# Optimization experiments

Measured on AMD Instinct MI355X. Metric: run time of the kernel, lower is better.

Reference implementation:

```python
import jax, jax.numpy as jnp
import numpy as np

CODEBOOK_SIZE = 65536
HIDDEN = 768
B, L = 2, 2048
COMMITMENT_COST = 0.25


def setup_inputs() -> dict:
    key = jax.random.key(0)
    k1, k2 = jax.random.split(key)
    embeddings = jax.random.normal(k1, (B, L, HIDDEN), dtype=jnp.float32)
    # torch init: uniform(-1/K, 1/K)
    bound = 1.0 / CODEBOOK_SIZE
    codebook = jax.random.uniform(k2, (CODEBOOK_SIZE, HIDDEN), dtype=jnp.float32,
                                  minval=-bound, maxval=bound)
    return {"embeddings": embeddings, "codebook": codebook}


def reference(embeddings, codebook):
    Bv, Lv, D = embeddings.shape
    z = embeddings.reshape(-1, D)  # (N, D)
    # pairwise squared distances: z^2 + e^2 - 2 z e^T  -> (N, K)
    z_sq = jnp.sum(z * z, axis=-1, keepdims=True)          # (N, 1)
    e_sq = jnp.sum(codebook * codebook, axis=-1)[None, :]  # (1, K)
    distances = z_sq + e_sq - 2.0 * (z @ codebook.T)       # (N, K)
    codes = jnp.argmin(distances, axis=-1)                 # (N,)
    quantized = codebook[codes]                            # (N, D) gather
    # VQ loss: codebook loss + commitment loss (stop-grads as in torch .detach())
    codebook_loss = jnp.mean((quantized - jax.lax.stop_gradient(z)) ** 2)
    commitment_loss = jnp.mean((z - jax.lax.stop_gradient(quantized)) ** 2)
    vq_loss = codebook_loss + COMMITMENT_COST * commitment_loss
    # straight-through estimator
    quantized_ste = z + jax.lax.stop_gradient(quantized - z)
    return (codes.reshape(Bv, Lv),
            quantized_ste.reshape(Bv, Lv, D),
            vq_loss)
```

## Files before the change

### kernel.cpp

```cpp
#include <hip/hip_runtime.h>
#include <cfloat>
#include <cstdint>

#define NROWS  4096
#define DIM    768
#define KCODES 65536

#define TM 128
#define TC 128
#define BK 64
#define SA 40
#define CAP 2048
#define DELTA 3.0e-4f

#define WS_ZSQ    0
#define WS_RUNMIN 16384
#define WS_CNT    32768
#define WS_CODESI 49152
#define WS_LOSS   65536
#define WS_LIST   131072
#define WS_AH     (WS_LIST + (size_t)NROWS*CAP*4)
#define WS_BH     (WS_AH + (size_t)NROWS*DIM*2)
#define WS_NEED   (WS_BH + (size_t)KCODES*DIM*2)

typedef _Float16 half_t;
typedef _Float16 half4 __attribute__((ext_vector_type(4)));
typedef _Float16 half8 __attribute__((ext_vector_type(8)));
typedef float    f32x4 __attribute__((ext_vector_type(4)));
typedef unsigned int uint;
typedef __attribute__((address_space(3))) half_t lds_half_t;

__device__ __forceinline__ void gld16(half_t* lds, const half_t* g) {
  __builtin_amdgcn_global_load_lds(
      (const __attribute__((address_space(1))) unsigned int*)g,
      (__attribute__((address_space(3))) unsigned int*)lds, 16, 0, 0);
}

__global__ void k_convA(const float* __restrict__ z, half_t* __restrict__ h,
                        float* __restrict__ zsq, unsigned int* __restrict__ runmin,
                        int* __restrict__ cnt, double* __restrict__ loss) {
  const int wave = threadIdx.x >> 6, lane = threadIdx.x & 63;
  const int row = blockIdx.x * 4 + wave;
  const float4* zr = (const float4*)(z + (size_t)row * DIM);
  half_t* hr = h + (size_t)row * DIM;
  float s = 0.f;
  #pragma unroll
  for (int p = 0; p < 3; ++p) {
    float4 v = zr[lane + p * 64];
    s = fmaf(v.x, v.x, s); s = fmaf(v.y, v.y, s);
    s = fmaf(v.z, v.z, s); s = fmaf(v.w, v.w, s);
    half4 hv = { (half_t)v.x, (half_t)v.y, (half_t)v.z, (half_t)v.w };
    *(half4*)(hr + (lane + p * 64) * 4) = hv;
  }
  #pragma unroll
  for (int off = 32; off; off >>= 1) s += __shfl_xor(s, off, 64);
  if (lane == 0) zsq[row] = s;
  const int gid = blockIdx.x * 256 + threadIdx.x;
  if (gid < NROWS) { runmin[gid] = 0x7f7fffffu; cnt[gid] = 0; }
  if (gid == 0) *loss = 0.0;
}

__global__ void k_convB(const float* __restrict__ src, half_t* __restrict__ h, int n8) {
  const int i = blockIdx.x * 256 + threadIdx.x;
  if (i >= n8) return;
  float4 v0 = ((const float4*)src)[2 * i];
  float4 v1 = ((const float4*)src)[2 * i + 1];
  float a[8] = {v0.x, v0.y, v0.z, v0.w, v1.x, v1.y, v1.z, v1.w};
  half8 hi;
  #pragma unroll
  for (int j = 0; j < 8; ++j) hi[j] = (half_t)(a[j] * 4096.f);
  ((half8*)h)[i] = hi;
}


#define GATE4 asm volatile("s_waitcnt vmcnt(4)" ::: "memory")
#define GATE0 asm volatile("s_waitcnt vmcnt(0)" ::: "memory")
#define GATEN
#define NOSTAGE

#define DSR(dst, base, imm) \
  asm volatile("ds_read_b128 %0, %1 offset:%2" : "=v"(dst) : "v"(base), "n"(imm))

#define MFMA2(AI, Ax0, Ax1, Bx0, Bx1) \
  acc[AI] = __builtin_amdgcn_mfma_f32_16x16x32_f16(Ax0, Bx0, acc[AI], 0, 0, 0); \
  acc[AI] = __builtin_amdgcn_mfma_f32_16x16x32_f16(Ax1, Bx1, acc[AI], 0, 0, 0)

#define STAGE_A(BUF, H, KD) { \
  gld16(stA + (BUF)*16384 + ((H)*128 +  0)*64, gAbase + (size_t)(((H)*64 +   0)*DIM) + (KD)); \
  gld16(stA + (BUF)*16384 + ((H)*128 + 64)*64, gAbase + (size_t)(((H)*64 + 128)*DIM) + (KD)); }

#define STAGE_B(BUF, G, KD) { \
  gld16(stB + (BUF)*16384 + ((G)*128 +  0)*64, gBbase + (size_t)(((G)*32 +   0)*DIM) + (KD)); \
  gld16(stB + (BUF)*16384 + ((G)*128 + 64)*64, gBbase + (size_t)(((G)*32 + 128)*DIM) + (KD)); }

#define PHASE_BODY(BUF, H, G, STAGE, GATE) { \
  half8 a00, a10, a20, a30, a01, a11, a21, a31, b00, b10, b01, b11; \
  DSR(a00, rA##BUF##0, (H)*16384 + 0); \
  DSR(a10, rA##BUF##0, (H)*16384 + 2048); \
  DSR(a20, rA##BUF##0, (H)*16384 + 4096); \
  DSR(a30, rA##BUF##0, (H)*16384 + 6144); \
  DSR(a01, rA##BUF##1, (H)*16384 + 0); \
  DSR(a11, rA##BUF##1, (H)*16384 + 2048); \
  DSR(a21, rA##BUF##1, (H)*16384 + 4096); \
  DSR(a31, rA##BUF##1, (H)*16384 + 6144); \
  DSR(b00, rB##BUF##0, (G)*16384 + 0); \
  DSR(b10, rB##BUF##0, (G)*16384 + 2048); \
  DSR(b01, rB##BUF##1, (G)*16384 + 0); \
  DSR(b11, rB##BUF##1, (G)*16384 + 2048); \
  STAGE; \
  __builtin_amdgcn_s_barrier(); \
  asm volatile("s_waitcnt lgkmcnt(0)" ::: "memory"); \
  __builtin_amdgcn_sched_barrier(0); \
  __builtin_amdgcn_s_setprio(1); \
  MFMA2(((H)*4+0)*4 + (G)*2 + 0, a00, a01, b00, b01); \
  MFMA2(((H)*4+0)*4 + (G)*2 + 1, a00, a01, b10, b11); \
  MFMA2(((H)*4+1)*4 + (G)*2 + 0, a10, a11, b00, b01); \
  MFMA2(((H)*4+1)*4 + (G)*2 + 1, a10, a11, b10, b11); \
  MFMA2(((H)*4+2)*4 + (G)*2 + 0, a20, a21, b00, b01); \
  MFMA2(((H)*4+2)*4 + (G)*2 + 1, a20, a21, b10, b11); \
  MFMA2(((H)*4+3)*4 + (G)*2 + 0, a30, a31, b00, b01); \
  MFMA2(((H)*4+3)*4 + (G)*2 + 1, a30, a31, b10, b11); \
  __builtin_amdgcn_s_setprio(0); \
  GATE; \
  __builtin_amdgcn_s_barrier(); }

__global__ __launch_bounds__(512, 2) void k1_s1(
    const half_t* __restrict__ Ahg, const half_t* __restrict__ Bhg,
    const float* __restrict__ zsq, unsigned int* __restrict__ runmin,
    int* __restrict__ cnt, int* __restrict__ list) {
  __shared__ __align__(16) half_t sA[2][256 * 64];
  __shared__ __align__(16) half_t sB[2][256 * 64];
  __shared__ float lzs[256];
  __shared__ float redD[256][4];
  __shared__ float lbound[256];

  const int tid = threadIdx.x;
  const int row0  = blockIdx.x * 256;
  const int code0 = blockIdx.y * 256;
  const int wave = tid >> 6, lane = tid & 63;
  const int wm = wave >> 2, wn = wave & 3;
  const int q = lane >> 4, l16 = lane & 15;
  const int sr = lane >> 3, ss = lane & 7;
  const int gsw8 = (ss ^ sr) * 8;
  const int s0 = wave * 8 + sr;

  if (tid < 256) lzs[tid] = zsq[row0 + tid];

  const uint ldsA = (uint)(size_t)(lds_half_t*)&sA[0][0];
  const uint ldsB = (uint)(size_t)(lds_half_t*)&sB[0][0];
  const int xr = l16 & 7;
  const uint rA00 = ldsA + (uint)((wm * 64 + l16) * 128 + ((q ^ xr) * 16));
  const uint rA01 = ldsA + (uint)((wm * 64 + l16) * 128 + (((4 + q) ^ xr) * 16));
  const uint rA10 = rA00 + 32768u;
  const uint rA11 = rA01 + 32768u;
  const uint rB00 = ldsB + (uint)((wn * 32 + l16) * 128 + ((q ^ xr) * 16));
  const uint rB01 = ldsB + (uint)((wn * 32 + l16) * 128 + (((4 + q) ^ xr) * 16));
  const uint rB10 = rB00 + 32768u;
  const uint rB11 = rB01 + 32768u;

  half_t* stA = &sA[0][0] + s0 * 64 + ss * 8;
  half_t* stB = &sB[0][0] + s0 * 64 + ss * 8;
  const half_t* gAbase = Ahg + (size_t)(row0 + s0) * DIM + gsw8;
  const half_t* gBbase = Bhg + (size_t)(code0 + (s0 >> 5) * 64 + (s0 & 31)) * DIM + gsw8;

  f32x4 acc[32];
  #pragma unroll
  for (int i = 0; i < 32; ++i) acc[i] = (f32x4){0.f, 0.f, 0.f, 0.f};

  STAGE_A(0, 0, 0);  STAGE_B(0, 1, 0);  STAGE_A(0, 1, 0);  STAGE_B(0, 0, 0);
  STAGE_A(1, 0, 64); STAGE_B(1, 1, 64);
  GATE4;
  asm volatile("s_waitcnt lgkmcnt(0)" ::: "memory");
  __builtin_amdgcn_s_barrier();

  for (int t = 0; t < 5; ++t) {
    const int kdB  = t * 128 + 64;
    const int kdN0 = t * 128 + 128;
    const int kdN1 = t * 128 + 192;
    PHASE_BODY(0, 0, 0, STAGE_A(1, 1, kdB),  GATEN);
    PHASE_BODY(0, 0, 1, STAGE_B(1, 0, kdB),  GATEN);
    PHASE_BODY(0, 1, 1, STAGE_A(0, 0, kdN0), GATEN);
    PHASE_BODY(0, 1, 0, STAGE_B(0, 1, kdN0), GATE4);
    PHASE_BODY(1, 0, 0, STAGE_A(0, 1, kdN0), GATEN);
    PHASE_BODY(1, 0, 1, STAGE_B(0, 0, kdN0), GATEN);
    PHASE_BODY(1, 1, 1, STAGE_A(1, 0, kdN1), GATEN);
    PHASE_BODY(1, 1, 0, STAGE_B(1, 1, kdN1), GATE4);
  }
  {
    PHASE_BODY(0, 0, 0, STAGE_A(1, 1, 704), GATEN);
    PHASE_BODY(0, 0, 1, STAGE_B(1, 0, 704), GATEN);
    PHASE_BODY(0, 1, 1, NOSTAGE, GATEN);
    PHASE_BODY(0, 1, 0, NOSTAGE, GATE0);
    PHASE_BODY(1, 0, 0, NOSTAGE, GATEN);
    PHASE_BODY(1, 0, 1, NOSTAGE, GATEN);
    PHASE_BODY(1, 1, 1, NOSTAGE, GATEN);
    PHASE_BODY(1, 1, 0, NOSTAGE, GATEN);
  }

  const float c2 = -4.8828125e-4f;
  #pragma unroll
  for (int tm = 0; tm < 8; ++tm)
    #pragma unroll
    for (int reg = 0; reg < 4; ++reg) {
      const float zs = lzs[wm * 128 + tm * 16 + q * 4 + reg];
      #pragma unroll
      for (int tn = 0; tn < 4; ++tn)
        acc[tm * 4 + tn][reg] = fmaf(c2, acc[tm * 4 + tn][reg], zs);
    }

  #pragma unroll
  for (int tm = 0; tm < 8; ++tm)
    #pragma unroll
    for (int reg = 0; reg < 4; ++reg) {
      float m = acc[tm * 4 + 0][reg];
      #pragma unroll
      for (int tn = 1; tn < 4; ++tn) m = fminf(m, acc[tm * 4 + tn][reg]);
      #pragma unroll
      for (int off = 8; off; off >>= 1) m = fminf(m, __shfl_xor(m, off, 64));
      if (l16 == 0) redD[wm * 128 + tm * 16 + q * 4 + reg][wn] = m;
    }
  __syncthreads();
  if (tid < 256) {
    const float lm = fminf(fminf(redD[tid][0], redD[tid][1]),
                           fminf(redD[tid][2], redD[tid][3]));
    const unsigned rg = runmin[row0 + tid];
    atomicMin(&runmin[row0 + tid], __float_as_uint(lm));
    lbound[tid] = fminf(lm, __uint_as_float(rg)) + DELTA;
  }
  __syncthreads();

  #pragma unroll
  for (int tm = 0; tm < 8; ++tm)
    #pragma unroll
    for (int reg = 0; reg < 4; ++reg) {
      const int row_b = wm * 128 + tm * 16 + q * 4 + reg;
      const float b = lbound[row_b];
      #pragma unroll
      for (int tn = 0; tn < 4; ++tn) {
        const float d = acc[tm * 4 + tn][reg];
        if (d <= b) {
          const int grow = row0 + row_b;
          const int pos = atomicAdd(&cnt[grow], 1);
          if (pos < CAP) list[(size_t)grow * CAP + pos] = code0 + wn * 64 + tn * 16 + l16;
        }
      }
    }
}

__global__ void k_refine(const float* __restrict__ z, const float* __restrict__ cb,
                         const float* __restrict__ zsq, const int* __restrict__ cnt,
                         const int* __restrict__ list, float* __restrict__ out_codes,
                         float* __restrict__ outq, double* __restrict__ loss) {
  const int r = blockIdx.x;
  const int tid = threadIdx.x, wave = tid >> 6, lane = tid & 63;
  __shared__ unsigned long long wbest[4];
  __shared__ double wsum[4];
  __shared__ int sidx;
  __shared__ __align__(16) float zsh[DIM];

  if (tid < DIM / 4) ((float4*)zsh)[tid] = ((const float4*)(z + (size_t)r * DIM))[tid];
  __syncthreads();

  int n = cnt[r]; if (n > CAP) n = CAP;
  const bool empty = (n == 0); if (empty) n = 1;
  const double zsd = (double)zsq[r];
  unsigned long long best = ~0ull;
  for (int ci = wave; ci < n; ci += 4) {
    const int idx = empty ? 0 : list[(size_t)r * CAP + ci];
    const float4* cr = (const float4*)(cb + (size_t)idx * DIM);
    double s = 0.0;
    #pragma unroll
    for (int p = 0; p < 3; ++p) {
      const float4 cv = cr[lane + p * 64];
      const float4 zv = ((const float4*)zsh)[lane + p * 64];
      s += (double)zv.x * cv.x + (double)zv.y * cv.y +
           (double)zv.z * cv.z + (double)zv.w * cv.w;
    }
    #pragma unroll
    for (int off = 32; off; off >>= 1) s += __shfl_xor(s, off, 64);
    const float d = (float)(zsd - 2.0 * s);
    const unsigned long long key =
        ((unsigned long long)__float_as_uint(d) << 32) | (unsigned)idx;
    if (key < best) best = key;
  }
  if (lane == 0) wbest[wave] = best;
  __syncthreads();
  if (tid == 0) {
    unsigned long long b = wbest[0];
    #pragma unroll
    for (int w = 1; w < 4; ++w) if (wbest[w] < b) b = wbest[w];
    const int idx = (int)(unsigned)(b & 0xffffffffull);
    sidx = idx;
    out_codes[r] = (float)idx;
  }
  __syncthreads();

  const int c = sidx;
  double ls = 0.0;
  #pragma unroll
  for (int j = 0; j < 3; ++j) {
    const int e = tid + j * 256;
    const float qx = cb[(size_t)c * DIM + e];
    const float zx = zsh[e];
    const float dd = qx - zx;
    outq[(size_t)r * DIM + e] = zx + dd;
    ls += (double)dd * (double)dd;
  }
  #pragma unroll
  for (int off = 32; off; off >>= 1) ls += __shfl_xor(ls, off, 64);
  if (lane == 0) wsum[wave] = ls;
  __syncthreads();
  if (tid == 0) atomicAdd(loss, wsum[0] + wsum[1] + wsum[2] + wsum[3]);
}

__global__ void k4_final(const double* __restrict__ loss, float* __restrict__ out) {
  float m = (float)(*loss / ((double)NROWS * (double)DIM));
  out[0] = m + 0.25f * m;
}

__global__ void k0_zsq(const float* __restrict__ z, float* __restrict__ zsq,
                       unsigned long long* __restrict__ keys, double* __restrict__ loss) {
  const int wave = threadIdx.x >> 6, lane = threadIdx.x & 63;
  const int row = blockIdx.x * 4 + wave;
  const float* zr = z + (size_t)row * DIM;
  float s = 0.f;
  #pragma unroll
  for (int i = 0; i < DIM / 64; ++i) { float v = zr[lane + i * 64]; s = fmaf(v, v, s); }
  #pragma unroll
  for (int off = 32; off; off >>= 1) s += __shfl_xor(s, off, 64);
  if (lane == 0) zsq[row] = s;
  const int gid = blockIdx.x * 256 + threadIdx.x;
  if (gid < NROWS) keys[gid] = ~0ull;
  if (gid == 0) *loss = 0.0;
}

__global__ __launch_bounds__(256, 2) void k1_mfma(
    const float* __restrict__ z, const float* __restrict__ cb,
    const float* __restrict__ zsq, unsigned long long* __restrict__ keys) {
  __shared__ half_t Ah[TM * SA], Al[TM * SA], Bh[TC * SA], Bl[TC * SA];
  __shared__ float lzs[TM];
  __shared__ float redD[TM][2];
  __shared__ int   redI[TM][2];

  const int tid  = threadIdx.x;
  const int row0  = blockIdx.x * TM;
  const int code0 = blockIdx.y * TC;
  const int wave = tid >> 6, lane = tid & 63;
  const int wm = wave & 1, wn = wave >> 1;
  const int q = lane >> 4, l16 = lane & 15;

  if (tid < TM) lzs[tid] = zsq[row0 + tid];

  const int srow = tid >> 2;
  const int sko  = (tid & 3) * 8;

  f32x4 acc0[16], acc1[16];
  #pragma unroll
  for (int i = 0; i < 16; ++i) {
    acc0[i] = (f32x4){0.f, 0.f, 0.f, 0.f};
    acc1[i] = (f32x4){0.f, 0.f, 0.f, 0.f};
  }

  const float* zp = z  + (size_t)row0  * DIM;
  const float* bp = cb + (size_t)code0 * DIM;

  for (int kd = 0; kd < DIM; kd += 32) {
    __syncthreads();
    #pragma unroll
    for (int s = 0; s < 2; ++s) {
      const int r = srow + s * 64;
      const float* srca = zp + (size_t)r * DIM + kd + sko;
      float4 v0 = *(const float4*)srca;
      float4 v1 = *(const float4*)(srca + 4);
      float a[8] = {v0.x, v0.y, v0.z, v0.w, v1.x, v1.y, v1.z, v1.w};
      half8 hi, lo;
      #pragma unroll
      for (int j = 0; j < 8; ++j) {
        half_t h = (half_t)a[j];
        hi[j] = h;
        lo[j] = (half_t)((a[j] - (float)h) * 4096.f);
      }
      *(half8*)&Ah[r * SA + sko] = hi;
      *(half8*)&Al[r * SA + sko] = lo;
      const float* srcb = bp + (size_t)r * DIM + kd + sko;
      v0 = *(const float4*)srcb; v1 = *(const float4*)(srcb + 4);
      float b[8] = {v0.x, v0.y, v0.z, v0.w, v1.x, v1.y, v1.z, v1.w};
      #pragma unroll
      for (int j = 0; j < 8; ++j) {
        float bs = b[j] * 4096.f;
        half_t h = (half_t)bs;
        hi[j] = h;
        lo[j] = (half_t)((bs - (float)h) * 4096.f);
      }
      *(half8*)&Bh[r * SA + sko] = hi;
      *(half8*)&Bl[r * SA + sko] = lo;
    }
    __syncthreads();

    half8 fa_h[4], fa_l[4], fb_h[4], fb_l[4];
    #pragma unroll
    for (int t = 0; t < 4; ++t) {
      const int ar = (wm * 64 + t * 16 + l16) * SA + q * 8;
      fa_h[t] = *(const half8*)&Ah[ar];
      fa_l[t] = *(const half8*)&Al[ar];
      const int br = (wn * 64 + t * 16 + l16) * SA + q * 8;
      fb_h[t] = *(const half8*)&Bh[br];
      fb_l[t] = *(const half8*)&Bl[br];
    }
    #pragma unroll
    for (int tm = 0; tm < 4; ++tm)
      #pragma unroll
      for (int tn = 0; tn < 4; ++tn) {
        const int i = tm * 4 + tn;
        acc0[i] = __builtin_amdgcn_mfma_f32_16x16x32_f16(fa_h[tm], fb_h[tn], acc0[i], 0, 0, 0);
        acc1[i] = __builtin_amdgcn_mfma_f32_16x16x32_f16(fa_l[tm], fb_h[tn], acc1[i], 0, 0, 0);
        acc1[i] = __builtin_amdgcn_mfma_f32_16x16x32_f16(fa_h[tm], fb_l[tn], acc1[i], 0, 0, 0);
      }
  }

  const float c1 = 2.44140625e-4f;
  const float c2 = -4.8828125e-4f;
  #pragma unroll
  for (int tm = 0; tm < 4; ++tm) {
    #pragma unroll
    for (int reg = 0; reg < 4; ++reg) {
      const int row_b = wm * 64 + tm * 16 + q * 4 + reg;
      const float zs = lzs[row_b];
      float bd = FLT_MAX; int bi = 0x7fffffff;
      #pragma unroll
      for (int tn = 0; tn < 4; ++tn) {
        const int i = tm * 4 + tn;
        float v = fmaf(c1, acc1[i][reg], acc0[i][reg]);
        float d = fmaf(c2, v, zs);
        const int ci = code0 + wn * 64 + tn * 16 + l16;
        if (d < bd || (d == bd && ci < bi)) { bd = d; bi = ci; }
      }
      #pragma unroll
      for (int off = 8; off; off >>= 1) {
        float od = __shfl_xor(bd, off, 64);
        int   oi = __shfl_xor(bi, off, 64);
        if (od < bd || (od == bd && oi < bi)) { bd = od; bi = oi; }
      }
      if (l16 == 0) { redD[row_b][wn] = bd; redI[row_b][wn] = bi; }
    }
  }
  __syncthreads();
  if (tid < TM) {
    float d0 = redD[tid][0]; int i0 = redI[tid][0];
    float d1 = redD[tid][1]; int i1 = redI[tid][1];
    if (d1 < d0 || (d1 == d0 && i1 < i0)) { d0 = d1; i0 = i1; }
    unsigned long long key = ((unsigned long long)__float_as_uint(d0) << 32) | (unsigned int)i0;
    atomicMin(&keys[row0 + tid], key);
  }
}

__global__ void k2_codes(const unsigned long long* __restrict__ keys,
                         float* __restrict__ out_codes, int* __restrict__ codes_i) {
  const int r = blockIdx.x * 256 + threadIdx.x;
  const int idx = (int)(unsigned int)(keys[r] & 0xffffffffull);
  out_codes[r] = (float)idx;
  codes_i[r] = idx;
}

__global__ void k3_quant_loss(const float* __restrict__ z, const float* __restrict__ cb,
                              const int* __restrict__ codes, float* __restrict__ outq,
                              double* __restrict__ loss) {
  const int gid = blockIdx.x * blockDim.x + threadIdx.x;
  const int e0 = gid * 4;
  const int row = e0 / DIM;
  const int col = e0 - row * DIM;
  const int c = codes[row];
  const float4 zv = *(const float4*)(z + e0);
  const float4 qv = *(const float4*)(cb + (size_t)c * DIM + col);
  float d0 = qv.x - zv.x, d1 = qv.y - zv.y, d2 = qv.z - zv.z, d3 = qv.w - zv.w;
  float4 ov = { zv.x + d0, zv.y + d1, zv.z + d2, zv.w + d3 };
  *(float4*)(outq + e0) = ov;
  double s = (double)(d0 * d0) + (double)(d1 * d1) + (double)(d2 * d2) + (double)(d3 * d3);
  #pragma unroll
  for (int off = 32; off; off >>= 1) s += __shfl_xor(s, off, 64);
  __shared__ double wsum[4];
  const int wave = threadIdx.x >> 6, lane = threadIdx.x & 63;
  if (lane == 0) wsum[wave] = s;
  __syncthreads();
  if (threadIdx.x == 0) atomicAdd(loss, wsum[0] + wsum[1] + wsum[2] + wsum[3]);
}

extern "C" void kernel_launch(void* const* d_in, const int* in_sizes, int n_in,
                              void* d_out, int out_size, void* d_ws, size_t ws_size,
                              hipStream_t stream) {
  const float* z  = (const float*)d_in[0];
  const float* cb = (const float*)d_in[1];
  float* out = (float*)d_out;
  char* ws = (char*)d_ws;
  float*  zsq = (float*)(ws + WS_ZSQ);
  unsigned int* runmin = (unsigned int*)(ws + WS_RUNMIN);
  int* cnt     = (int*)(ws + WS_CNT);
  int* codes_i = (int*)(ws + WS_CODESI);
  double* loss = (double*)(ws + WS_LOSS);
  int* list    = (int*)(ws + WS_LIST);
  unsigned long long* keys = (unsigned long long*)(ws + WS_LIST);

  if (ws_size >= WS_NEED) {
    half_t* Ahg = (half_t*)(ws + WS_AH);
    half_t* Bhg = (half_t*)(ws + WS_BH);
    dim3 g1s(NROWS / 256, KCODES / 256);
    k_convA<<<NROWS / 4, 256, 0, stream>>>(z, Ahg, zsq, runmin, cnt, loss);
    k_convB<<<(KCODES * DIM / 8 + 255) / 256, 256, 0, stream>>>(cb, Bhg, KCODES * DIM / 8);
    k1_s1<<<g1s, 512, 0, stream>>>(Ahg, Bhg, zsq, runmin, cnt, list);
    k_refine<<<NROWS, 256, 0, stream>>>(z, cb, zsq, cnt, list, out, out + NROWS, loss);
  } else {
    dim3 g1(NROWS / TM, KCODES / TC);
    k0_zsq<<<NROWS / 4, 256, 0, stream>>>(z, zsq, keys, loss);
    k1_mfma<<<g1, 256, 0, stream>>>(z, cb, zsq, keys);
    k2_codes<<<NROWS / 256, 256, 0, stream>>>(keys, out, codes_i);
    k3_quant_loss<<<(NROWS * DIM / 4) / 256, 256, 0, stream>>>(z, cb, codes_i, out + NROWS, loss);
  }

  k4_final<<<1, 1, 0, stream>>>(loss, out + NROWS + (size_t)NROWS * DIM);
}
```

Baseline: 1.000 ms.

## Reuse A/B fragments across GEMM phases and prefetch next fragments before barrier

The main distance-GEMM loop now keeps A and B LDS fragments in persistent registers and orders the four quadrant phases so each phase reloads only the half that changes, either A or B. Before, every phase re-read all 12 fragments from LDS. The next fragments are issued after the MFMAs and before the trailing barrier, so LDS reads overlap the barrier wait. This cuts LDS read traffic and issue slots, but the prefetch reads must land before the next phase's stage writes, and it may raise register pressure.

```diff
diff --git a/kernel.cpp b/kernel.cpp
--- a/kernel.cpp
+++ b/kernel.cpp
@@ -77,9 +77,26 @@
 #define GATE0 asm volatile("s_waitcnt vmcnt(0)" ::: "memory")
 #define GATEN
 #define NOSTAGE
+#define NORD
 
 #define DSR(dst, base, imm) \
   asm volatile("ds_read_b128 %0, %1 offset:%2" : "=v"(dst) : "v"(base), "n"(imm))
+
+#define RD_FA(BUF, H) { \
+  DSR(fa0, rA00, (BUF)*32768 + (H)*16384 + 0); \
+  DSR(fa1, rA01, (BUF)*32768 + (H)*16384 + 0); \
+  DSR(fa2, rA00, (BUF)*32768 + (H)*16384 + 2048); \
+  DSR(fa3, rA01, (BUF)*32768 + (H)*16384 + 2048); \
+  DSR(fa4, rA00, (BUF)*32768 + (H)*16384 + 4096); \
+  DSR(fa5, rA01, (BUF)*32768 + (H)*16384 + 4096); \
+  DSR(fa6, rA00, (BUF)*32768 + (H)*16384 + 6144); \
+  DSR(fa7, rA01, (BUF)*32768 + (H)*16384 + 6144); }
+
+#define RD_FB(BUF, G) { \
+  DSR(fb0, rB00, (BUF)*32768 + (G)*16384 + 0); \
+  DSR(fb1, rB01, (BUF)*32768 + (G)*16384 + 0); \
+  DSR(fb2, rB00, (BUF)*32768 + (G)*16384 + 2048); \
+  DSR(fb3, rB01, (BUF)*32768 + (G)*16384 + 2048); }
 
 #define MFMA2(AI, Ax0, Ax1, Bx0, Bx1) \
   acc[AI] = __builtin_amdgcn_mfma_f32_16x16x32_f16(Ax0, Bx0, acc[AI], 0, 0, 0); \
@@ -93,35 +110,25 @@
   gld16(stB + (BUF)*16384 + ((G)*128 +  0)*64, gBbase + (size_t)(((G)*32 +   0)*DIM) + (KD)); \
   gld16(stB + (BUF)*16384 + ((G)*128 + 64)*64, gBbase + (size_t)(((G)*32 + 128)*DIM) + (KD)); }
 
-#define PHASE_BODY(BUF, H, G, STAGE, GATE) { \
-  half8 a00, a10, a20, a30, a01, a11, a21, a31, b00, b10, b01, b11; \
-  DSR(a00, rA##BUF##0, (H)*16384 + 0); \
-  DSR(a10, rA##BUF##0, (H)*16384 + 2048); \
-  DSR(a20, rA##BUF##0, (H)*16384 + 4096); \
-  DSR(a30, rA##BUF##0, (H)*16384 + 6144); \
-  DSR(a01, rA##BUF##1, (H)*16384 + 0); \
-  DSR(a11, rA##BUF##1, (H)*16384 + 2048); \
-  DSR(a21, rA##BUF##1, (H)*16384 + 4096); \
-  DSR(a31, rA##BUF##1, (H)*16384 + 6144); \
-  DSR(b00, rB##BUF##0, (G)*16384 + 0); \
-  DSR(b10, rB##BUF##0, (G)*16384 + 2048); \
-  DSR(b01, rB##BUF##1, (G)*16384 + 0); \
-  DSR(b11, rB##BUF##1, (G)*16384 + 2048); \
+#define PHASE(H, G, STARTRD, STAGE, GATE, POSTRD) { \
+  STARTRD; \
   STAGE; \
   __builtin_amdgcn_s_barrier(); \
   asm volatile("s_waitcnt lgkmcnt(0)" ::: "memory"); \
   __builtin_amdgcn_sched_barrier(0); \
   __builtin_amdgcn_s_setprio(1); \
-  MFMA2(((H)*4+0)*4 + (G)*2 + 0, a00, a01, b00, b01); \
-  MFMA2(((H)*4+0)*4 + (G)*2 + 1, a00, a01, b10, b11); \
-  MFMA2(((H)*4+1)*4 + (G)*2 + 0, a10, a11, b00, b01); \
-  MFMA2(((H)*4+1)*4 + (G)*2 + 1, a10, a11, b10, b11); \
-  MFMA2(((H)*4+2)*4 + (G)*2 + 0, a20, a21, b00, b01); \
-  MFMA2(((H)*4+2)*4 + (G)*2 + 1, a20, a21, b10, b11); \
-  MFMA2(((H)*4+3)*4 + (G)*2 + 0, a30, a31, b00, b01); \
-  MFMA2(((H)*4+3)*4 + (G)*2 + 1, a30, a31, b10, b11); \
+  MFMA2(((H)*4+0)*4 + (G)*2 + 0, fa0, fa1, fb0, fb1); \
+  MFMA2(((H)*4+0)*4 + (G)*2 + 1, fa0, fa1, fb2, fb3); \
+  MFMA2(((H)*4+1)*4 + (G)*2 + 0, fa2, fa3, fb0, fb1); \
+  MFMA2(((H)*4+1)*4 + (G)*2 + 1, fa2, fa3, fb2, fb3); \
+  MFMA2(((H)*4+2)*4 + (G)*2 + 0, fa4, fa5, fb0, fb1); \
+  MFMA2(((H)*4+2)*4 + (G)*2 + 1, fa4, fa5, fb2, fb3); \
+  MFMA2(((H)*4+3)*4 + (G)*2 + 0, fa6, fa7, fb0, fb1); \
+  MFMA2(((H)*4+3)*4 + (G)*2 + 1, fa6, fa7, fb2, fb3); \
   __builtin_amdgcn_s_setprio(0); \
+  __builtin_amdgcn_sched_barrier(0); \
   GATE; \
+  POSTRD; \
   __builtin_amdgcn_s_barrier(); }
 
 __global__ __launch_bounds__(512, 2) void k1_s1(
@@ -151,17 +158,16 @@
   const int xr = l16 & 7;
   const uint rA00 = ldsA + (uint)((wm * 64 + l16) * 128 + ((q ^ xr) * 16));
   const uint rA01 = ldsA + (uint)((wm * 64 + l16) * 128 + (((4 + q) ^ xr) * 16));
-  const uint rA10 = rA00 + 32768u;
-  const uint rA11 = rA01 + 32768u;
   const uint rB00 = ldsB + (uint)((wn * 32 + l16) * 128 + ((q ^ xr) * 16));
   const uint rB01 = ldsB + (uint)((wn * 32 + l16) * 128 + (((4 + q) ^ xr) * 16));
-  const uint rB10 = rB00 + 32768u;
-  const uint rB11 = rB01 + 32768u;
 
   half_t* stA = &sA[0][0] + s0 * 64 + ss * 8;
   half_t* stB = &sB[0][0] + s0 * 64 + ss * 8;
   const half_t* gAbase = Ahg + (size_t)(row0 + s0) * DIM + gsw8;
   const half_t* gBbase = Bhg + (size_t)(code0 + (s0 >> 5) * 64 + (s0 & 31)) * DIM + gsw8;
+
+  half8 fa0, fa1, fa2, fa3, fa4, fa5, fa6, fa7;
+  half8 fb0, fb1, fb2, fb3;
 
   f32x4 acc[32];
   #pragma unroll
@@ -177,24 +183,24 @@
     const int kdB  = t * 128 + 64;
     const int kdN0 = t * 128 + 128;
     const int kdN1 = t * 128 + 192;
-    PHASE_BODY(0, 0, 0, STAGE_A(1, 1, kdB),  GATEN);
-    PHASE_BODY(0, 0, 1, STAGE_B(1, 0, kdB),  GATEN);
-    PHASE_BODY(0, 1, 1, STAGE_A(0, 0, kdN0), GATEN);
-    PHASE_BODY(0, 1, 0, STAGE_B(0, 1, kdN0), GATE4);
-    PHASE_BODY(1, 0, 0, STAGE_A(0, 1, kdN0), GATEN);
-    PHASE_BODY(1, 0, 1, STAGE_B(0, 0, kdN0), GATEN);
-    PHASE_BODY(1, 1, 1, STAGE_A(1, 0, kdN1), GATEN);
-    PHASE_BODY(1, 1, 0, STAGE_B(1, 1, kdN1), GATE4);
+    PHASE(0, 0, { RD_FA(0,0); RD_FB(0,0); }, STAGE_A(1, 1, kdB),  GATEN, RD_FB(0,1));
+    PHASE(0, 1, NORD,                        STAGE_B(1, 0, kdB),  GATEN, RD_FA(0,1));
+    PHASE(1, 1, NORD,                        STAGE_A(0, 0, kdN0), GATEN, RD_FB(0,0));
+    PHASE(1, 0, NORD,                        STAGE_B(0, 1, kdN0), GATE4, NORD);
+    PHASE(0, 0, { RD_FA(1,0); RD_FB(1,0); }, STAGE_A(0, 1, kdN0), GATEN, RD_FB(1,1));
+    PHASE(0, 1, NORD,                        STAGE_B(0, 0, kdN0), GATEN, RD_FA(1,1));
+    PHASE(1, 1, NORD,                        STAGE_A(1, 0, kdN1), GATEN, RD_FB(1,0));
+    PHASE(1, 0, NORD,                        STAGE_B(1, 1, kdN1), GATE4, NORD);
   }
   {
-    PHASE_BODY(0, 0, 0, STAGE_A(1, 1, 704), GATEN);
-    PHASE_BODY(0, 0, 1, STAGE_B(1, 0, 704), GATEN);
-    PHASE_BODY(0, 1, 1, NOSTAGE, GATEN);
-    PHASE_BODY(0, 1, 0, NOSTAGE, GATE0);
-    PHASE_BODY(1, 0, 0, NOSTAGE, GATEN);
-    PHASE_BODY(1, 0, 1, NOSTAGE, GATEN);
-    PHASE_BODY(1, 1, 1, NOSTAGE, GATEN);
-    PHASE_BODY(1, 1, 0, NOSTAGE, GATEN);
+    PHASE(0, 0, { RD_FA(0,0); RD_FB(0,0); }, STAGE_A(1, 1, 704), GATEN, RD_FB(0,1));
+    PHASE(0, 1, NORD,                        STAGE_B(1, 0, 704), GATEN, RD_FA(0,1));
+    PHASE(1, 1, NORD,                        NOSTAGE,            GATEN, RD_FB(0,0));
+    PHASE(1, 0, NORD,                        NOSTAGE,            GATE0, NORD);
+    PHASE(0, 0, { RD_FA(1,0); RD_FB(1,0); }, NOSTAGE,            GATEN, RD_FB(1,1));
+    PHASE(0, 1, NORD,                        NOSTAGE,            GATEN, RD_FA(1,1));
+    PHASE(1, 1, NORD,                        NOSTAGE,            GATEN, RD_FB(1,0));
+    PHASE(1, 0, NORD,                        NOSTAGE,            GATEN, NORD);
   }
 
   const float c2 = -4.8828125e-4f;
```

Result: faster. 950.7 us (-4.9%).
